# Kernel optimization log

Measured on AMD Instinct MI355X. Metric: run time of the kernel, lower is better.

Reference implementation:

```python
import jax, jax.numpy as jnp
import numpy as np

BLOCK_SIZE = 256
N_EMBED = 384
HEAD_SIZE = 64


def setup_inputs() -> dict:
    key = jax.random.key(0)
    kx, kq, kk, kv = jax.random.split(key, 4)
    B, T = 256, 256
    x = jax.random.normal(kx, (B, T, N_EMBED), dtype=jnp.float32)
    # nn.Linear(n_embed, head_size, bias=False): y = x @ W.T with W [head, embed].
    # We store the transposed weight [embed, head] so forward is x @ W.
    scale = 1.0 / np.sqrt(N_EMBED)
    Wq = jax.random.normal(kq, (N_EMBED, HEAD_SIZE), dtype=jnp.float32) * scale
    Wk = jax.random.normal(kk, (N_EMBED, HEAD_SIZE), dtype=jnp.float32) * scale
    Wv = jax.random.normal(kv, (N_EMBED, HEAD_SIZE), dtype=jnp.float32) * scale
    return {"x": x, "Wq": Wq, "Wk": Wk, "Wv": Wv}


def reference(x, Wq, Wk, Wv):
    B, T, C = x.shape  # C == N_EMBED
    q = jnp.einsum('btc,ch->bth', x, Wq)
    k = jnp.einsum('btc,ch->bth', x, Wk)
    v = jnp.einsum('btc,ch->bth', x, Wv)
    # NOTE: original scales by 1/sqrt(C) where C = embed dim (384), not head_size.
    wei = jnp.einsum('bth,bsh->bts', q, k) / jnp.sqrt(jnp.float32(C))
    causal = jnp.tril(jnp.ones((T, T), dtype=bool))
    wei = jnp.where(causal, wei, -jnp.inf)
    wei = jax.nn.softmax(wei, axis=-1)
    # dropout is identity in eval mode (reference is deterministic)
    out = jnp.einsum('bts,bsh->bth', wei, v)
    return out
```

## Files before the change

kernel.cpp:

```cpp
#include <hip/hip_runtime.h>


typedef short s16x8 __attribute__((ext_vector_type(8)));
typedef float f32x4 __attribute__((ext_vector_type(4)));
typedef float f32x2 __attribute__((ext_vector_type(2)));
typedef unsigned u32x4 __attribute__((ext_vector_type(4)));
typedef __bf16 bf16x2t __attribute__((ext_vector_type(2)));

#define MFMA16(a, b, c) __builtin_amdgcn_mfma_f32_16x16x32_bf16((a), (b), (c), 0, 0, 0)

__device__ __forceinline__ unsigned short f2bf(float f) {
  return __builtin_bit_cast(unsigned short, (__bf16)f);
}
__device__ __forceinline__ unsigned cvt2(float a, float b) {
  f32x2 t; t[0] = a; t[1] = b;
  bf16x2t r = __builtin_convertvector(t, bf16x2t);
  return __builtin_bit_cast(unsigned, r);
}
__device__ __forceinline__ s16x8 cvt8(float4 a, float4 b) {
  u32x4 u;
  u[0] = cvt2(a.x, a.y); u[1] = cvt2(a.z, a.w);
  u[2] = cvt2(b.x, b.y); u[3] = cvt2(b.z, b.w);
  return __builtin_bit_cast(s16x8, u);
}

__global__ __launch_bounds__(256) void wcvt(
    const float* __restrict__ Wq, const float* __restrict__ Wk,
    const float* __restrict__ Wv, unsigned short* __restrict__ Wt_sw) {
  int idx = blockIdx.x * 256 + threadIdx.x;
  int j = idx & 7;
  int c = idx >> 3;
  int n15 = c & 15;
  int q4 = (c >> 4) & 3;
  int g = c >> 6;
  int nt = g % 12;
  int kc = g / 12;
  int n = nt * 16 + n15;
  int kk = kc * 32 + q4 * 8 + j;
  const float* src = (n < 64) ? Wq : (n < 128) ? Wk : Wv;
  float v = src[kk * 64 + (n & 63)];
  if (n < 64) v *= 0.05103103630798287f;
  Wt_sw[idx] = f2bf(v);
}

__global__ __launch_bounds__(256, 2) void qkv_proj(
    const float* __restrict__ x, const unsigned short* __restrict__ Wt_sw,
    unsigned short* __restrict__ q_sw, unsigned short* __restrict__ k_sw,
    unsigned short* __restrict__ v_sw) {
  const int tid = threadIdx.x;
  const int lane = tid & 63;
  const int wv = tid >> 6;
  const int n15 = lane & 15;
  const int q4 = lane >> 4;
  const long row0 = (long)blockIdx.x * 128 + wv * 32;

  f32x4 acc[12][2];
#pragma unroll
  for (int i = 0; i < 12; ++i)
#pragma unroll
    for (int t = 0; t < 2; ++t) acc[i][t] = (f32x4){0.f, 0.f, 0.f, 0.f};

  const float* xp0 = x + (row0 + n15) * 384 + q4 * 8;
  const float* xp1 = x + (row0 + 16 + n15) * 384 + q4 * 8;
  float4 c00 = *reinterpret_cast<const float4*>(xp0);
  float4 c01 = *reinterpret_cast<const float4*>(xp0 + 4);
  float4 c10 = *reinterpret_cast<const float4*>(xp1);
  float4 c11 = *reinterpret_cast<const float4*>(xp1 + 4);

  s16x8 wc[12];
#pragma unroll
  for (int nt = 0; nt < 12; ++nt)
    wc[nt] = *reinterpret_cast<const s16x8*>(Wt_sw + nt * 512 + lane * 8);

  for (int kc = 0; kc < 12; ++kc) {
    const int nkc = (kc < 11) ? kc + 1 : 11;
    float4 p00 = *reinterpret_cast<const float4*>(xp0 + nkc * 32);
    float4 p01 = *reinterpret_cast<const float4*>(xp0 + nkc * 32 + 4);
    float4 p10 = *reinterpret_cast<const float4*>(xp1 + nkc * 32);
    float4 p11 = *reinterpret_cast<const float4*>(xp1 + nkc * 32 + 4);
    s16x8 wn[12];
#pragma unroll
    for (int nt = 0; nt < 12; ++nt)
      wn[nt] = *reinterpret_cast<const s16x8*>(Wt_sw + (nkc * 12 + nt) * 512 + lane * 8);

    s16x8 xa[2];
    xa[0] = cvt8(c00, c01);
    xa[1] = cvt8(c10, c11);

#pragma unroll
    for (int nt = 0; nt < 12; ++nt) {
#pragma unroll
      for (int t = 0; t < 2; ++t) {
        if (nt < 8) acc[nt][t] = MFMA16(wc[nt], xa[t], acc[nt][t]);
        else        acc[nt][t] = MFMA16(xa[t], wc[nt], acc[nt][t]);
      }
    }
    c00 = p00; c01 = p01; c10 = p10; c11 = p11;
#pragma unroll
    for (int nt = 0; nt < 12; ++nt) wc[nt] = wn[nt];
  }

  const long bb_ = row0 >> 8;
  unsigned short* qb = q_sw + bb_ * 16384;
  unsigned short* kb = k_sw + bb_ * 16384;
  unsigned short* vb = v_sw + bb_ * 16384;
#pragma unroll
  for (int t = 0; t < 2; ++t) {
    const int rb = (int)(row0 & 255) + t * 16;
    const int qtile = rb >> 4;
#pragma unroll
    for (int mt = 0; mt < 4; ++mt) {
      const int off = ((qtile * 2 + (mt >> 1)) * 64 + (2 * (mt & 1) + (q4 >> 1)) * 16 + n15) * 8
                      + (q4 & 1) * 4;
      uint2 sq, sk;
      sq.x = cvt2(acc[mt][t][0], acc[mt][t][1]);
      sq.y = cvt2(acc[mt][t][2], acc[mt][t][3]);
      sk.x = cvt2(acc[4 + mt][t][0], acc[4 + mt][t][1]);
      sk.y = cvt2(acc[4 + mt][t][2], acc[4 + mt][t][3]);
      *reinterpret_cast<uint2*>(qb + off) = sq;
      *reinterpret_cast<uint2*>(kb + off) = sk;
    }
    const int s0 = rb + q4 * 4;
#pragma unroll
    for (int nt = 0; nt < 4; ++nt) {
      const int off = (((s0 >> 5) * 4 + nt) * 64 + ((s0 >> 3) & 3) * 16 + n15) * 8 + (s0 & 7);
      uint2 sv;
      sv.x = cvt2(acc[8 + nt][t][0], acc[8 + nt][t][1]);
      sv.y = cvt2(acc[8 + nt][t][2], acc[8 + nt][t][3]);
      *reinterpret_cast<uint2*>(vb + off) = sv;
    }
  }
}

__global__ __launch_bounds__(256) void attn(
    const unsigned short* __restrict__ q_sw, const unsigned short* __restrict__ k_sw,
    const unsigned short* __restrict__ v_sw, float* __restrict__ out) {
  const int b = blockIdx.x & 255;
  const int j = blockIdx.x >> 8;
  const int tid = threadIdx.x;
  const int wv = tid >> 6;
  const int lane = tid & 63;
  const int n15 = lane & 15;
  const int q4 = lane >> 4;

  const int qt = (wv == 0) ? j : (wv == 1) ? 7 - j : (wv == 2) ? 8 + j : 15 - j;

  const unsigned short* qb = q_sw + b * 16384;
  const unsigned short* kb = k_sw + b * 16384;
  const unsigned short* vb = v_sw + b * 16384;

  const s16x8 qf0 = *reinterpret_cast<const s16x8*>(qb + (qt * 2 + 0) * 512 + lane * 8);
  const s16x8 qf1 = *reinterpret_cast<const s16x8*>(qb + (qt * 2 + 1) * 512 + lane * 8);

  uint2 pk[16];
  float psum = 0.f;
  s16x8 kf0 = *reinterpret_cast<const s16x8*>(kb + 0 * 512 + lane * 8);
  s16x8 kf1 = *reinterpret_cast<const s16x8*>(kb + 1 * 512 + lane * 8);
#pragma unroll 16
  for (int ct = 0; ct < 16; ++ct) {
    if (ct > qt) break;
    const int nc = (ct < qt) ? ct + 1 : ct;
    s16x8 nf0 = *reinterpret_cast<const s16x8*>(kb + (nc * 2 + 0) * 512 + lane * 8);
    s16x8 nf1 = *reinterpret_cast<const s16x8*>(kb + (nc * 2 + 1) * 512 + lane * 8);
    f32x4 a = (f32x4){0.f, 0.f, 0.f, 0.f};
    a = MFMA16(kf0, qf0, a);
    a = MFMA16(kf1, qf1, a);
    const bool diag = (ct == qt);
    float p[4];
#pragma unroll
    for (int e = 0; e < 4; ++e) {
      p[e] = (diag && (q4 * 4 + e > n15)) ? 0.f : __expf(a[e]);
      psum += p[e];
    }
    pk[ct].x = cvt2(p[0], p[1]);
    pk[ct].y = cvt2(p[2], p[3]);
    kf0 = nf0; kf1 = nf1;
  }
  psum += __shfl_xor(psum, 16);
  psum += __shfl_xor(psum, 32);
  const float rn_col = 1.0f / psum;

  f32x4 O[4];
#pragma unroll
  for (int nt = 0; nt < 4; ++nt) O[nt] = (f32x4){0.f, 0.f, 0.f, 0.f};
  const int nk = (qt + 2) >> 1;
  s16x8 vf[4], vn[4];
#pragma unroll
  for (int nt = 0; nt < 4; ++nt)
    vf[nt] = *reinterpret_cast<const s16x8*>(vb + nt * 512 + lane * 8);
  const int laneA = ((q4 & 1) << 5) + n15;
  const bool hi = (q4 >> 1) != 0;
#pragma unroll 8
  for (int kc = 0; kc < 8; ++kc) {
    if (kc >= nk) break;
    const int ncc = (kc + 1 < nk) ? kc + 1 : kc;
#pragma unroll
    for (int nt = 0; nt < 4; ++nt)
      vn[nt] = *reinterpret_cast<const s16x8*>(vb + (ncc * 4 + nt) * 512 + lane * 8);
    const uint2 t0 = pk[2 * kc];
    const uint2 t1 = (2 * kc + 1 <= qt) ? pk[2 * kc + 1] : make_uint2(0u, 0u);
    unsigned r0a = __shfl(t0.x, laneA),      r0b = __shfl(t0.y, laneA);
    unsigned r0c = __shfl(t0.x, laneA + 16), r0d = __shfl(t0.y, laneA + 16);
    unsigned r1a = __shfl(t1.x, laneA),      r1b = __shfl(t1.y, laneA);
    unsigned r1c = __shfl(t1.x, laneA + 16), r1d = __shfl(t1.y, laneA + 16);
    u32x4 u;
    u[0] = hi ? r1a : r0a; u[1] = hi ? r1b : r0b;
    u[2] = hi ? r1c : r0c; u[3] = hi ? r1d : r0d;
    s16x8 pf = __builtin_bit_cast(s16x8, u);
#pragma unroll
    for (int nt = 0; nt < 4; ++nt) {
      O[nt] = MFMA16(pf, vf[nt], O[nt]);
      vf[nt] = vn[nt];
    }
  }
  float rnm[4];
#pragma unroll
  for (int e = 0; e < 4; ++e) rnm[e] = __shfl(rn_col, q4 * 4 + e);
#pragma unroll
  for (int nt = 0; nt < 4; ++nt)
#pragma unroll
    for (int e = 0; e < 4; ++e)
      out[(size_t)(b * 256 + qt * 16 + q4 * 4 + e) * 64 + nt * 16 + n15] = O[nt][e] * rnm[e];
}

extern "C" void kernel_launch(void* const* d_in, const int* in_sizes, int n_in,
                              void* d_out, int out_size, void* d_ws, size_t ws_size,
                              hipStream_t stream) {
  const float* x  = (const float*)d_in[0];
  const float* Wq = (const float*)d_in[1];
  const float* Wk = (const float*)d_in[2];
  const float* Wv = (const float*)d_in[3];
  float* out = (float*)d_out;

  unsigned short* q_sw = (unsigned short*)d_ws;
  unsigned short* k_sw = q_sw + (size_t)65536 * 64;
  unsigned short* v_sw = k_sw + (size_t)65536 * 64;
  unsigned short* Wt_sw = v_sw + (size_t)65536 * 64;

  wcvt<<<288, 256, 0, stream>>>(Wq, Wk, Wv, Wt_sw);
  qkv_proj<<<512, 256, 0, stream>>>(x, Wt_sw, q_sw, k_sw, v_sw);
  attn<<<1024, 256, 0, stream>>>(q_sw, k_sw, v_sw, out);
}
```

Baseline: 201.6 us.

## Fuse QKV projection and causal attention into one kernel using LDS

Merges the projection and attention kernels into a single 512-thread kernel per batch. Q, K and V for a batch go to shared memory instead of global workspace, and each wave then handles two query tiles, paired so that causal work is balanced. This removes the global round trip for Q/K/V and one launch. In exchange the grid drops to 256 blocks using 96KB of LDS each, which lowers occupancy and overlap, and there is a barrier between the phases.

```diff
diff --git a/kernel.cpp b/kernel.cpp
--- a/kernel.cpp
+++ b/kernel.cpp
@@ -43,184 +43,173 @@
   Wt_sw[idx] = f2bf(v);
 }
 
-__global__ __launch_bounds__(256, 2) void qkv_proj(
+__global__ __launch_bounds__(512) void fused_attn(
     const float* __restrict__ x, const unsigned short* __restrict__ Wt_sw,
-    unsigned short* __restrict__ q_sw, unsigned short* __restrict__ k_sw,
-    unsigned short* __restrict__ v_sw) {
-  const int tid = threadIdx.x;
-  const int lane = tid & 63;
-  const int wv = tid >> 6;
-  const int n15 = lane & 15;
-  const int q4 = lane >> 4;
-  const long row0 = (long)blockIdx.x * 128 + wv * 32;
-
-  f32x4 acc[12][2];
-#pragma unroll
-  for (int i = 0; i < 12; ++i)
-#pragma unroll
-    for (int t = 0; t < 2; ++t) acc[i][t] = (f32x4){0.f, 0.f, 0.f, 0.f};
-
-  const float* xp0 = x + (row0 + n15) * 384 + q4 * 8;
-  const float* xp1 = x + (row0 + 16 + n15) * 384 + q4 * 8;
-  float4 c00 = *reinterpret_cast<const float4*>(xp0);
-  float4 c01 = *reinterpret_cast<const float4*>(xp0 + 4);
-  float4 c10 = *reinterpret_cast<const float4*>(xp1);
-  float4 c11 = *reinterpret_cast<const float4*>(xp1 + 4);
-
-  s16x8 wc[12];
-#pragma unroll
-  for (int nt = 0; nt < 12; ++nt)
-    wc[nt] = *reinterpret_cast<const s16x8*>(Wt_sw + nt * 512 + lane * 8);
-
-  for (int kc = 0; kc < 12; ++kc) {
-    const int nkc = (kc < 11) ? kc + 1 : 11;
-    float4 p00 = *reinterpret_cast<const float4*>(xp0 + nkc * 32);
-    float4 p01 = *reinterpret_cast<const float4*>(xp0 + nkc * 32 + 4);
-    float4 p10 = *reinterpret_cast<const float4*>(xp1 + nkc * 32);
-    float4 p11 = *reinterpret_cast<const float4*>(xp1 + nkc * 32 + 4);
-    s16x8 wn[12];
-#pragma unroll
-    for (int nt = 0; nt < 12; ++nt)
-      wn[nt] = *reinterpret_cast<const s16x8*>(Wt_sw + (nkc * 12 + nt) * 512 + lane * 8);
-
-    s16x8 xa[2];
-    xa[0] = cvt8(c00, c01);
-    xa[1] = cvt8(c10, c11);
-
-#pragma unroll
-    for (int nt = 0; nt < 12; ++nt) {
-#pragma unroll
-      for (int t = 0; t < 2; ++t) {
-        if (nt < 8) acc[nt][t] = MFMA16(wc[nt], xa[t], acc[nt][t]);
-        else        acc[nt][t] = MFMA16(xa[t], wc[nt], acc[nt][t]);
-      }
-    }
-    c00 = p00; c01 = p01; c10 = p10; c11 = p11;
-#pragma unroll
-    for (int nt = 0; nt < 12; ++nt) wc[nt] = wn[nt];
-  }
-
-  const long bb_ = row0 >> 8;
-  unsigned short* qb = q_sw + bb_ * 16384;
-  unsigned short* kb = k_sw + bb_ * 16384;
-  unsigned short* vb = v_sw + bb_ * 16384;
-#pragma unroll
-  for (int t = 0; t < 2; ++t) {
-    const int rb = (int)(row0 & 255) + t * 16;
-    const int qtile = rb >> 4;
-#pragma unroll
-    for (int mt = 0; mt < 4; ++mt) {
-      const int off = ((qtile * 2 + (mt >> 1)) * 64 + (2 * (mt & 1) + (q4 >> 1)) * 16 + n15) * 8
-                      + (q4 & 1) * 4;
-      uint2 sq, sk;
-      sq.x = cvt2(acc[mt][t][0], acc[mt][t][1]);
-      sq.y = cvt2(acc[mt][t][2], acc[mt][t][3]);
-      sk.x = cvt2(acc[4 + mt][t][0], acc[4 + mt][t][1]);
-      sk.y = cvt2(acc[4 + mt][t][2], acc[4 + mt][t][3]);
-      *reinterpret_cast<uint2*>(qb + off) = sq;
-      *reinterpret_cast<uint2*>(kb + off) = sk;
-    }
-    const int s0 = rb + q4 * 4;
-#pragma unroll
-    for (int nt = 0; nt < 4; ++nt) {
-      const int off = (((s0 >> 5) * 4 + nt) * 64 + ((s0 >> 3) & 3) * 16 + n15) * 8 + (s0 & 7);
-      uint2 sv;
-      sv.x = cvt2(acc[8 + nt][t][0], acc[8 + nt][t][1]);
-      sv.y = cvt2(acc[8 + nt][t][2], acc[8 + nt][t][3]);
-      *reinterpret_cast<uint2*>(vb + off) = sv;
-    }
-  }
-}
-
-__global__ __launch_bounds__(256) void attn(
-    const unsigned short* __restrict__ q_sw, const unsigned short* __restrict__ k_sw,
-    const unsigned short* __restrict__ v_sw, float* __restrict__ out) {
-  const int b = blockIdx.x & 255;
-  const int j = blockIdx.x >> 8;
+    float* __restrict__ out) {
+  __shared__ unsigned short q_l[16384];
+  __shared__ unsigned short k_l[16384];
+  __shared__ unsigned short v_l[16384];
+  const int b = blockIdx.x;
   const int tid = threadIdx.x;
   const int wv = tid >> 6;
   const int lane = tid & 63;
   const int n15 = lane & 15;
   const int q4 = lane >> 4;
 
-  const int qt = (wv == 0) ? j : (wv == 1) ? 7 - j : (wv == 2) ? 8 + j : 15 - j;
-
-  const unsigned short* qb = q_sw + b * 16384;
-  const unsigned short* kb = k_sw + b * 16384;
-  const unsigned short* vb = v_sw + b * 16384;
-
-  const s16x8 qf0 = *reinterpret_cast<const s16x8*>(qb + (qt * 2 + 0) * 512 + lane * 8);
-  const s16x8 qf1 = *reinterpret_cast<const s16x8*>(qb + (qt * 2 + 1) * 512 + lane * 8);
-
-  uint2 pk[16];
-  float psum = 0.f;
-  s16x8 kf0 = *reinterpret_cast<const s16x8*>(kb + 0 * 512 + lane * 8);
-  s16x8 kf1 = *reinterpret_cast<const s16x8*>(kb + 1 * 512 + lane * 8);
-#pragma unroll 16
-  for (int ct = 0; ct < 16; ++ct) {
-    if (ct > qt) break;
-    const int nc = (ct < qt) ? ct + 1 : ct;
-    s16x8 nf0 = *reinterpret_cast<const s16x8*>(kb + (nc * 2 + 0) * 512 + lane * 8);
-    s16x8 nf1 = *reinterpret_cast<const s16x8*>(kb + (nc * 2 + 1) * 512 + lane * 8);
-    f32x4 a = (f32x4){0.f, 0.f, 0.f, 0.f};
-    a = MFMA16(kf0, qf0, a);
-    a = MFMA16(kf1, qf1, a);
-    const bool diag = (ct == qt);
-    float p[4];
-#pragma unroll
-    for (int e = 0; e < 4; ++e) {
-      p[e] = (diag && (q4 * 4 + e > n15)) ? 0.f : __expf(a[e]);
-      psum += p[e];
-    }
-    pk[ct].x = cvt2(p[0], p[1]);
-    pk[ct].y = cvt2(p[2], p[3]);
-    kf0 = nf0; kf1 = nf1;
+  {
+    const int rb0 = wv * 32;
+    f32x4 acc[12][2];
+#pragma unroll
+    for (int i = 0; i < 12; ++i)
+#pragma unroll
+      for (int t = 0; t < 2; ++t) acc[i][t] = (f32x4){0.f, 0.f, 0.f, 0.f};
+
+    const float* xp0 = x + ((long)b * 256 + rb0 + n15) * 384 + q4 * 8;
+    const float* xp1 = xp0 + 16 * 384;
+    float4 c00 = *reinterpret_cast<const float4*>(xp0);
+    float4 c01 = *reinterpret_cast<const float4*>(xp0 + 4);
+    float4 c10 = *reinterpret_cast<const float4*>(xp1);
+    float4 c11 = *reinterpret_cast<const float4*>(xp1 + 4);
+
+    s16x8 wc[12];
+#pragma unroll
+    for (int nt = 0; nt < 12; ++nt)
+      wc[nt] = *reinterpret_cast<const s16x8*>(Wt_sw + nt * 512 + lane * 8);
+
+    for (int kc = 0; kc < 12; ++kc) {
+      const int nkc = (kc < 11) ? kc + 1 : 11;
+      float4 p00 = *reinterpret_cast<const float4*>(xp0 + nkc * 32);
+      float4 p01 = *reinterpret_cast<const float4*>(xp0 + nkc * 32 + 4);
+      float4 p10 = *reinterpret_cast<const float4*>(xp1 + nkc * 32);
+      float4 p11 = *reinterpret_cast<const float4*>(xp1 + nkc * 32 + 4);
+      s16x8 wn[12];
+#pragma unroll
+      for (int nt = 0; nt < 12; ++nt)
+        wn[nt] = *reinterpret_cast<const s16x8*>(Wt_sw + (nkc * 12 + nt) * 512 + lane * 8);
+
+      s16x8 xa[2];
+      xa[0] = cvt8(c00, c01);
+      xa[1] = cvt8(c10, c11);
+
+#pragma unroll
+      for (int nt = 0; nt < 12; ++nt) {
+#pragma unroll
+        for (int t = 0; t < 2; ++t) {
+          if (nt < 8) acc[nt][t] = MFMA16(wc[nt], xa[t], acc[nt][t]);
+          else        acc[nt][t] = MFMA16(xa[t], wc[nt], acc[nt][t]);
+        }
+      }
+      c00 = p00; c01 = p01; c10 = p10; c11 = p11;
+#pragma unroll
+      for (int nt = 0; nt < 12; ++nt) wc[nt] = wn[nt];
+    }
+
+#pragma unroll
+    for (int t = 0; t < 2; ++t) {
+      const int rb = rb0 + t * 16;
+      const int qtile = rb >> 4;
+#pragma unroll
+      for (int mt = 0; mt < 4; ++mt) {
+        const int off = ((qtile * 2 + (mt >> 1)) * 64 + (2 * (mt & 1) + (q4 >> 1)) * 16 + n15) * 8
+                        + (q4 & 1) * 4;
+        uint2 sq, sk;
+        sq.x = cvt2(acc[mt][t][0], acc[mt][t][1]);
+        sq.y = cvt2(acc[mt][t][2], acc[mt][t][3]);
+        sk.x = cvt2(acc[4 + mt][t][0], acc[4 + mt][t][1]);
+        sk.y = cvt2(acc[4 + mt][t][2], acc[4 + mt][t][3]);
+        *reinterpret_cast<uint2*>(&q_l[off]) = sq;
+        *reinterpret_cast<uint2*>(&k_l[off]) = sk;
+      }
+      const int s0 = rb + q4 * 4;
+#pragma unroll
+      for (int nt = 0; nt < 4; ++nt) {
+        const int off = (((s0 >> 5) * 4 + nt) * 64 + ((s0 >> 3) & 3) * 16 + n15) * 8 + (s0 & 7);
+        uint2 sv;
+        sv.x = cvt2(acc[8 + nt][t][0], acc[8 + nt][t][1]);
+        sv.y = cvt2(acc[8 + nt][t][2], acc[8 + nt][t][3]);
+        *reinterpret_cast<uint2*>(&v_l[off]) = sv;
+      }
+    }
   }
-  psum += __shfl_xor(psum, 16);
-  psum += __shfl_xor(psum, 32);
-  const float rn_col = 1.0f / psum;
-
-  f32x4 O[4];
-#pragma unroll
-  for (int nt = 0; nt < 4; ++nt) O[nt] = (f32x4){0.f, 0.f, 0.f, 0.f};
-  const int nk = (qt + 2) >> 1;
-  s16x8 vf[4], vn[4];
-#pragma unroll
-  for (int nt = 0; nt < 4; ++nt)
-    vf[nt] = *reinterpret_cast<const s16x8*>(vb + nt * 512 + lane * 8);
+  __syncthreads();
+
   const int laneA = ((q4 & 1) << 5) + n15;
   const bool hi = (q4 >> 1) != 0;
+#pragma unroll
+  for (int half = 0; half < 2; ++half) {
+    const int qt = half ? (15 - wv) : wv;
+
+    const s16x8 qf0 = *reinterpret_cast<const s16x8*>(&q_l[(qt * 2 + 0) * 512 + lane * 8]);
+    const s16x8 qf1 = *reinterpret_cast<const s16x8*>(&q_l[(qt * 2 + 1) * 512 + lane * 8]);
+
+    uint2 pk[16];
+    float psum = 0.f;
+    s16x8 kf0 = *reinterpret_cast<const s16x8*>(&k_l[0 * 512 + lane * 8]);
+    s16x8 kf1 = *reinterpret_cast<const s16x8*>(&k_l[1 * 512 + lane * 8]);
+#pragma unroll 16
+    for (int ct = 0; ct < 16; ++ct) {
+      if (ct > qt) break;
+      const int nc = (ct < qt) ? ct + 1 : ct;
+      s16x8 nf0 = *reinterpret_cast<const s16x8*>(&k_l[(nc * 2 + 0) * 512 + lane * 8]);
+      s16x8 nf1 = *reinterpret_cast<const s16x8*>(&k_l[(nc * 2 + 1) * 512 + lane * 8]);
+      f32x4 a = (f32x4){0.f, 0.f, 0.f, 0.f};
+      a = MFMA16(kf0, qf0, a);
+      a = MFMA16(kf1, qf1, a);
+      const bool diag = (ct == qt);
+      float p[4];
+#pragma unroll
+      for (int e = 0; e < 4; ++e) {
+        p[e] = (diag && (q4 * 4 + e > n15)) ? 0.f : __expf(a[e]);
+        psum += p[e];
+      }
+      pk[ct].x = cvt2(p[0], p[1]);
+      pk[ct].y = cvt2(p[2], p[3]);
+      kf0 = nf0; kf1 = nf1;
+    }
+    psum += __shfl_xor(psum, 16);
+    psum += __shfl_xor(psum, 32);
+    const float rn_col = 1.0f / psum;
+
+    f32x4 O[4];
+#pragma unroll
+    for (int nt = 0; nt < 4; ++nt) O[nt] = (f32x4){0.f, 0.f, 0.f, 0.f};
+    const int nk = (qt + 2) >> 1;
+    s16x8 vf[4], vn[4];
+#pragma unroll
+    for (int nt = 0; nt < 4; ++nt)
+      vf[nt] = *reinterpret_cast<const s16x8*>(&v_l[nt * 512 + lane * 8]);
 #pragma unroll 8
-  for (int kc = 0; kc < 8; ++kc) {
-    if (kc >= nk) break;
-    const int ncc = (kc + 1 < nk) ? kc + 1 : kc;
+    for (int kc = 0; kc < 8; ++kc) {
+      if (kc >= nk) break;
+      const int ncc = (kc + 1 < nk) ? kc + 1 : kc;
+#pragma unroll
+      for (int nt = 0; nt < 4; ++nt)
+        vn[nt] = *reinterpret_cast<const s16x8*>(&v_l[(ncc * 4 + nt) * 512 + lane * 8]);
+      const uint2 t0 = pk[2 * kc];
+      const uint2 t1 = (2 * kc + 1 <= qt) ? pk[2 * kc + 1] : make_uint2(0u, 0u);
+      unsigned r0a = __shfl(t0.x, laneA),      r0b = __shfl(t0.y, laneA);
+      unsigned r0c = __shfl(t0.x, laneA + 16), r0d = __shfl(t0.y, laneA + 16);
+      unsigned r1a = __shfl(t1.x, laneA),      r1b = __shfl(t1.y, laneA);
+      unsigned r1c = __shfl(t1.x, laneA + 16), r1d = __shfl(t1.y, laneA + 16);
+      u32x4 u;
+      u[0] = hi ? r1a : r0a; u[1] = hi ? r1b : r0b;
+      u[2] = hi ? r1c : r0c; u[3] = hi ? r1d : r0d;
+      s16x8 pf = __builtin_bit_cast(s16x8, u);
+#pragma unroll
+      for (int nt = 0; nt < 4; ++nt) {
+        O[nt] = MFMA16(pf, vf[nt], O[nt]);
+        vf[nt] = vn[nt];
+      }
+    }
+    float rnm[4];
+#pragma unroll
+    for (int e = 0; e < 4; ++e) rnm[e] = __shfl(rn_col, q4 * 4 + e);
 #pragma unroll
     for (int nt = 0; nt < 4; ++nt)
-      vn[nt] = *reinterpret_cast<const s16x8*>(vb + (ncc * 4 + nt) * 512 + lane * 8);
-    const uint2 t0 = pk[2 * kc];
-    const uint2 t1 = (2 * kc + 1 <= qt) ? pk[2 * kc + 1] : make_uint2(0u, 0u);
-    unsigned r0a = __shfl(t0.x, laneA),      r0b = __shfl(t0.y, laneA);
-    unsigned r0c = __shfl(t0.x, laneA + 16), r0d = __shfl(t0.y, laneA + 16);
-    unsigned r1a = __shfl(t1.x, laneA),      r1b = __shfl(t1.y, laneA);
-    unsigned r1c = __shfl(t1.x, laneA + 16), r1d = __shfl(t1.y, laneA + 16);
-    u32x4 u;
-    u[0] = hi ? r1a : r0a; u[1] = hi ? r1b : r0b;
-    u[2] = hi ? r1c : r0c; u[3] = hi ? r1d : r0d;
-    s16x8 pf = __builtin_bit_cast(s16x8, u);
-#pragma unroll
-    for (int nt = 0; nt < 4; ++nt) {
-      O[nt] = MFMA16(pf, vf[nt], O[nt]);
-      vf[nt] = vn[nt];
-    }
+#pragma unroll
+      for (int e = 0; e < 4; ++e)
+        out[(size_t)(b * 256 + qt * 16 + q4 * 4 + e) * 64 + nt * 16 + n15] = O[nt][e] * rnm[e];
   }
-  float rnm[4];
-#pragma unroll
-  for (int e = 0; e < 4; ++e) rnm[e] = __shfl(rn_col, q4 * 4 + e);
-#pragma unroll
-  for (int nt = 0; nt < 4; ++nt)
-#pragma unroll
-    for (int e = 0; e < 4; ++e)
-      out[(size_t)(b * 256 + qt * 16 + q4 * 4 + e) * 64 + nt * 16 + n15] = O[nt][e] * rnm[e];
 }
 
 extern "C" void kernel_launch(void* const* d_in, const int* in_sizes, int n_in,
@@ -232,12 +221,8 @@
   const float* Wv = (const float*)d_in[3];
   float* out = (float*)d_out;
 
-  unsigned short* q_sw = (unsigned short*)d_ws;
-  unsigned short* k_sw = q_sw + (size_t)65536 * 64;
-  unsigned short* v_sw = k_sw + (size_t)65536 * 64;
-  unsigned short* Wt_sw = v_sw + (size_t)65536 * 64;
+  unsigned short* Wt_sw = (unsigned short*)d_ws;
 
   wcvt<<<288, 256, 0, stream>>>(Wq, Wk, Wv, Wt_sw);
-  qkv_proj<<<512, 256, 0, stream>>>(x, Wt_sw, q_sw, k_sw, v_sw);
-  attn<<<1024, 256, 0, stream>>>(q_sw, k_sw, v_sw, out);
-}
+  fused_attn<<<256, 512, 0, stream>>>(x, Wt_sw, out);
+}
```

New measurement: 193.9 us. 3.8% less time.
